# Optimization experiments

Hardware: AMD Instinct MI355X
Metric: run time of the kernel (lower is better)

The kernel has to match this reference:

```python
import jax, jax.numpy as jnp
import numpy as np

B, S, E, H, FFN, NQ = 4, 2048, 1024, 16, 4096, 8
DK = E // H
EPS = 1e-5


def setup_inputs() -> dict:
    key = jax.random.key(0)
    ks = jax.random.split(key, 8)
    x = jax.random.normal(ks[0], (B, S, E), dtype=jnp.float32)
    theta = jax.random.normal(ks[1], (NQ,), dtype=jnp.float32)  # RY angles
    w1 = jax.random.normal(ks[2], (FFN, NQ), dtype=jnp.float32) / np.sqrt(NQ)
    b1 = jnp.zeros((FFN,), dtype=jnp.float32)
    w2 = jax.random.normal(ks[3], (E, FFN), dtype=jnp.float32) / np.sqrt(FFN)
    b2 = jnp.zeros((E,), dtype=jnp.float32)
    gamma1 = jnp.ones((E,), dtype=jnp.float32)
    beta1 = jnp.zeros((E,), dtype=jnp.float32)
    gamma2 = jnp.ones((E,), dtype=jnp.float32)
    beta2 = jnp.zeros((E,), dtype=jnp.float32)
    return {"x": x, "theta": theta, "w1": w1, "b1": b1, "w2": w2, "b2": b2,
            "gamma1": gamma1, "beta1": beta1, "gamma2": gamma2, "beta2": beta2}


def _layernorm(h, g, b):
    mu = jnp.mean(h, axis=-1, keepdims=True)
    var = jnp.mean(jnp.square(h - mu), axis=-1, keepdims=True)
    return (h - mu) * jax.lax.rsqrt(var + EPS) * g + b


def _attention(x):
    # q = k = v = separate_heads(x); no projection weights in the original.
    q = x.reshape(B, S, H, DK).transpose(0, 2, 1, 3)  # [B,H,S,DK]
    scores = jnp.einsum("bhqd,bhkd->bhqk", q, q) / np.sqrt(DK)
    probs = jax.nn.softmax(scores, axis=-1)
    out = jnp.einsum("bhqk,bhkd->bhqd", probs, q)
    return out.transpose(0, 2, 1, 3).reshape(B, S, E)


def _ffn_quantum(h, theta, w1, b1, w2, b2):
    # Per-token circuit: RX(x_i) then RY(theta_i) on independent qubits,
    # measure PauliZ -> <Z_i> = cos(x_i) * cos(theta_i). Batched over all tokens.
    qout = jnp.cos(h[..., :NQ]) * jnp.cos(theta)  # [B,S,NQ]
    hid = jax.nn.relu(jnp.einsum("bsq,fq->bsf", qout, w1) + b1)
    return jnp.einsum("bsf,ef->bse", hid, w2) + b2


def reference(x, theta, w1, b1, w2, b2, gamma1, beta1, gamma2, beta2):
    attn_out = _attention(x)
    h = _layernorm(x + attn_out, gamma1, beta1)
    ffn_out = _ffn_quantum(h, theta, w1, b1, w2, b2)
    return _layernorm(h + ffn_out, gamma2, beta2)
```

## Files before the change

kernel.cpp:

```cpp
#include <hip/hip_runtime.h>


#define Bq 4
#define Sq 2048
#define Eq 1024
#define Hq 16
#define DKq 64
#define FFNq 4096
#define NQq 8
#define LOG2E 1.44269504f

typedef unsigned int u32;
typedef unsigned short u16;
typedef _Float16 f16;
typedef f16 f16x8 __attribute__((ext_vector_type(8)));
typedef __fp16 fp16x2 __attribute__((ext_vector_type(2)));
typedef float f32x4 __attribute__((ext_vector_type(4)));
typedef u32 u32x2 __attribute__((ext_vector_type(2)));
typedef u32 u32x4 __attribute__((ext_vector_type(4)));

#if __has_builtin(__builtin_amdgcn_exp2f)
#define EXP2F __builtin_amdgcn_exp2f
#else
#define EXP2F exp2f
#endif

#define MFMA(a, b, c) __builtin_amdgcn_mfma_f32_16x16x32_f16((a), (b), (c), 0, 0, 0)

#define GLL(g, l)                                                          \
  __builtin_amdgcn_global_load_lds(                                        \
      (const __attribute__((address_space(1))) u32*)(g),                   \
      (__attribute__((address_space(3))) u32*)(l), 16, 0, 0)

__device__ __forceinline__ u16 f2h(float x) {
  f16 t = (f16)x;
  return __builtin_bit_cast(u16, t);
}
__device__ __forceinline__ float h2f(u16 w) {
  return (float)__builtin_bit_cast(f16, w);
}
#if __has_builtin(__builtin_amdgcn_cvt_pkrtz)
__device__ __forceinline__ u32 pkrtz(float a, float b) {
  fp16x2 r = __builtin_amdgcn_cvt_pkrtz(a, b);
  return __builtin_bit_cast(u32, r);
}
#else
__device__ __forceinline__ u32 pkrtz(float a, float b) {
  return (u32)f2h(a) | ((u32)f2h(b) << 16);
}
#endif

__device__ __forceinline__ void swap32(u32 a, u32 b, u32& r0, u32& r1) {
#if __has_builtin(__builtin_amdgcn_permlane32_swap)
  u32x2 r = __builtin_amdgcn_permlane32_swap(a, b, false, false);
  r0 = r[0];
  r1 = r[1];
#else
  u32 ax = (u32)__shfl_xor((int)a, 32);
  u32 bx = (u32)__shfl_xor((int)b, 32);
  const bool lo = (threadIdx.x & 32) == 0;
  r0 = lo ? a : bx;
  r1 = lo ? ax : b;
#endif
}

union F8 { f16x8 v; u32 w[4]; u16 h[8]; f16 e[8]; };

__global__ void k_cvt(const float* __restrict__ src, uint4* __restrict__ dst, int n8) {
  int i = blockIdx.x * 256 + threadIdx.x;
  if (i >= n8) return;
  const float4* s = (const float4*)src + 2 * (long)i;
  float4 a = s[0], b = s[1];
  uint4 r;
  r.x = pkrtz(a.x, a.y);
  r.y = pkrtz(a.z, a.w);
  r.z = pkrtz(b.x, b.y);
  r.w = pkrtz(b.z, b.w);
  dst[i] = r;
}

__global__ void k_prep(const float* __restrict__ x, u16* __restrict__ xh,
                       u16* __restrict__ xt) {
  __shared__ u16 tile[64 * 72];
  const int tid = threadIdx.x;
  const int bx = blockIdx.x;
  const int sb = bx & 31, bh = bx >> 5;
  const int b = bh >> 4, h = bh & 15;
  const int s0 = sb * 64;
  const int r = tid >> 2, cq = tid & 3;
  const float* xp = x + ((long)(b * Sq + s0 + r)) * Eq + h * 64 + cq * 16;
  float4 f0 = ((const float4*)xp)[0], f1 = ((const float4*)xp)[1];
  float4 f2 = ((const float4*)xp)[2], f3 = ((const float4*)xp)[3];
  u32 w[8];
  w[0] = pkrtz(f0.x, f0.y); w[1] = pkrtz(f0.z, f0.w);
  w[2] = pkrtz(f1.x, f1.y); w[3] = pkrtz(f1.z, f1.w);
  w[4] = pkrtz(f2.x, f2.y); w[5] = pkrtz(f2.z, f2.w);
  w[6] = pkrtz(f3.x, f3.y); w[7] = pkrtz(f3.z, f3.w);
  uint4* xo = (uint4*)(xh + ((long)(b * Sq + s0 + r)) * Eq + h * 64 + cq * 16);
  xo[0] = make_uint4(w[0], w[1], w[2], w[3]);
  xo[1] = make_uint4(w[4], w[5], w[6], w[7]);
  uint4* tp = (uint4*)(tile + r * 72 + cq * 16);
  tp[0] = make_uint4(w[0], w[1], w[2], w[3]);
  tp[1] = make_uint4(w[4], w[5], w[6], w[7]);
  __syncthreads();
  const int d = tid >> 2, rq = tid & 3;
  u32 o[8];
#pragma unroll
  for (int i = 0; i < 8; ++i) {
    u32 lo = tile[(rq * 16 + 2 * i) * 72 + d];
    u32 hi = tile[(rq * 16 + 2 * i + 1) * 72 + d];
    o[i] = lo | (hi << 16);
  }
  uint4* to = (uint4*)(xt + ((long)(bh * 64 + d)) * Sq + s0 + rq * 16);
  to[0] = make_uint4(o[0], o[1], o[2], o[3]);
  to[1] = make_uint4(o[4], o[5], o[6], o[7]);
}

__global__ __launch_bounds__(512, 4) void k_attn(const u16* __restrict__ xh,
                                                 const u16* __restrict__ xt,
                                                 u16* __restrict__ attn) {
  __shared__ __align__(16) u16 lds[16384];

  const int tid = threadIdx.x;
  const int wave = tid >> 6, lane = tid & 63;
  const int n = lane & 15, quad = lane >> 4;
  const bool quadEven = (quad & 1) == 0;

  const int bx = blockIdx.x;
  const int qb = bx >> 6, bh = bx & 63;
  const int b = bh >> 4, h = bh & 15;

  const u16* xh_bh = xh + (long)b * Sq * Eq + h * 64;
  const u16* xt_bh = xt + (long)bh * 64 * Sq;

  const float SC = 0.125f * LOG2E;
  F8 qf[2][2];
  float shift[2], lrow[2] = {0.f, 0.f};
#pragma unroll
  for (int nt = 0; nt < 2; ++nt) {
    const int q = qb * 256 + wave * 32 + nt * 16 + n;
    const u16* qp = xh_bh + (long)q * Eq + quad * 8;
    F8 a, c;
    a.v = *(const f16x8*)qp;
    c.v = *(const f16x8*)(qp + 32);
    float s2 = 0.f;
#pragma unroll
    for (int i = 0; i < 8; ++i) {
      float va = (float)a.e[i], vc = (float)c.e[i];
      s2 += va * va + vc * vc;
      qf[nt][0].e[i] = a.e[i] * (f16)SC;
      qf[nt][1].e[i] = c.e[i] * (f16)SC;
    }
    s2 += __shfl_xor(s2, 16);
    s2 += __shfl_xor(s2, 32);
    shift[nt] = SC * s2;
  }

  const int r8 = lane >> 3;
  const int cl = (lane & 7) ^ r8;
  const u16* gK = xh_bh + (long)(wave * 8 + r8) * Eq + cl * 8;
  const u16* gV = xt_bh + (long)(wave * 8 + r8) * Sq + cl * 8;
  const int lK = wave * 512;
  const int lV = 4096 + wave * 512;

  u16* cur = lds;
  u16* nxt = lds + 8192;

  GLL(gK, cur + lK);
  GLL(gV, cur + lV);
  gK += 64 * Eq;
  gV += 64;

  f32x4 O[2][4] = {};

  for (int kb = 0; kb < Sq / 64; ++kb) {
    __syncthreads();
    if (kb < Sq / 64 - 1) {
      GLL(gK, nxt + lK);
      GLL(gV, nxt + lV);
      gK += 64 * Eq;
      gV += 64;
    }
    u16* Kl = cur;
    u16* Vt = cur + 4096;

    f32x4 ST[2][4];
#pragma unroll
    for (int nt = 0; nt < 2; ++nt) {
      const float ms = -shift[nt];
#pragma unroll
      for (int mt = 0; mt < 4; ++mt) {
        ST[nt][mt][0] = ms; ST[nt][mt][1] = ms;
        ST[nt][mt][2] = ms; ST[nt][mt][3] = ms;
      }
    }
    __builtin_amdgcn_s_setprio(1);
#pragma unroll
    for (int mt = 0; mt < 4; ++mt) {
#pragma unroll
      for (int c = 0; c < 2; ++c) {
        f16x8 af = *(const f16x8*)(Kl + (mt * 16 + n) * 64 +
                                   (((c * 4 + quad) ^ (n & 7)) * 8));
#pragma unroll
        for (int nt = 0; nt < 2; ++nt)
          ST[nt][mt] = MFMA(af, qf[nt][c].v, ST[nt][mt]);
      }
    }
    __builtin_amdgcn_s_setprio(0);

    f16x8 pfr[2][2];
#pragma unroll
    for (int nt = 0; nt < 2; ++nt) {
      u32 pk[8];
      float ls = 0.f;
#pragma unroll
      for (int mt = 0; mt < 4; ++mt) {
        float p0 = EXP2F(ST[nt][mt][0]);
        float p1 = EXP2F(ST[nt][mt][1]);
        float p2 = EXP2F(ST[nt][mt][2]);
        float p3 = EXP2F(ST[nt][mt][3]);
        ls += (p0 + p1) + (p2 + p3);
        pk[2 * mt] = pkrtz(p0, p1);
        pk[2 * mt + 1] = pkrtz(p2, p3);
      }
      lrow[nt] += ls;
#pragma unroll
      for (int c = 0; c < 2; ++c) {
        u32 r00, r10, r01, r11;
        swap32(pk[4 * c + 0], pk[4 * c + 2], r00, r10);
        swap32(pk[4 * c + 1], pk[4 * c + 3], r01, r11);
        u32 U0 = quadEven ? r10 : r00;
        u32 U1 = quadEven ? r11 : r01;
        u32 Ux0 = (u32)__shfl_xor((int)U0, 16);
        u32 Ux1 = (u32)__shfl_xor((int)U1, 16);
        u32x4 wv;
        wv[0] = quadEven ? r00 : Ux0;
        wv[1] = quadEven ? r01 : Ux1;
        wv[2] = quadEven ? Ux0 : r10;
        wv[3] = quadEven ? Ux1 : r11;
        pfr[nt][c] = __builtin_bit_cast(f16x8, wv);
      }
    }

    __builtin_amdgcn_s_setprio(1);
#pragma unroll
    for (int c = 0; c < 2; ++c) {
      const int pc = ((c * 4 + quad) ^ (n & 7)) * 8;
#pragma unroll
      for (int dt = 0; dt < 4; ++dt) {
        f16x8 vf = *(const f16x8*)(Vt + (dt * 16 + n) * 64 + pc);
#pragma unroll
        for (int nt = 0; nt < 2; ++nt) O[nt][dt] = MFMA(vf, pfr[nt][c], O[nt][dt]);
      }
    }
    __builtin_amdgcn_s_setprio(0);
    u16* t = cur; cur = nxt; nxt = t;
  }

#pragma unroll
  for (int nt = 0; nt < 2; ++nt) {
    float l = lrow[nt];
    l += __shfl_xor(l, 16);
    l += __shfl_xor(l, 32);
    const float inv = 1.0f / l;
    const int q = qb * 256 + wave * 32 + nt * 16 + n;
    u16* op = attn + (long)b * Sq * Eq + (long)q * Eq + h * 64;
#pragma unroll
    for (int dt = 0; dt < 4; ++dt) {
      u32 w0 = pkrtz(O[nt][dt][0] * inv, O[nt][dt][1] * inv);
      u32 w1 = pkrtz(O[nt][dt][2] * inv, O[nt][dt][3] * inv);
      *(uint2*)(op + dt * 16 + quad * 4) = make_uint2(w0, w1);
    }
  }
}

__global__ void k_ln1(const u16* __restrict__ xh, const u16* __restrict__ attn,
                      const float* __restrict__ g, const float* __restrict__ be,
                      const float* __restrict__ theta, u16* __restrict__ hout,
                      u16* __restrict__ qout) {
  const long t = blockIdx.x;
  const int tid = threadIdx.x;
  uint2 xw = ((const uint2*)(xh + t * Eq))[tid];
  uint2 aw = ((const uint2*)(attn + t * Eq))[tid];
  float v0 = h2f(xw.x & 0xffff) + h2f(aw.x & 0xffff);
  float v1 = h2f(xw.x >> 16) + h2f(aw.x >> 16);
  float v2 = h2f(xw.y & 0xffff) + h2f(aw.y & 0xffff);
  float v3 = h2f(xw.y >> 16) + h2f(aw.y >> 16);
  float s = (v0 + v1) + (v2 + v3);
  float s2 = v0 * v0 + v1 * v1 + v2 * v2 + v3 * v3;
#pragma unroll
  for (int o = 1; o < 64; o <<= 1) {
    s += __shfl_xor(s, o);
    s2 += __shfl_xor(s2, o);
  }
  __shared__ float red[8];
  const int wv = tid >> 6, ln = tid & 63;
  if (ln == 0) { red[wv] = s; red[4 + wv] = s2; }
  __syncthreads();
  s = red[0] + red[1] + red[2] + red[3];
  s2 = red[4] + red[5] + red[6] + red[7];
  const float mu = s * (1.f / Eq);
  const float var = s2 * (1.f / Eq) - mu * mu;
  const float rstd = rsqrtf(var + 1e-5f);
  float4 gv = ((const float4*)g)[tid];
  float4 bv = ((const float4*)be)[tid];
  float o0 = (v0 - mu) * rstd * gv.x + bv.x;
  float o1 = (v1 - mu) * rstd * gv.y + bv.y;
  float o2 = (v2 - mu) * rstd * gv.z + bv.z;
  float o3 = (v3 - mu) * rstd * gv.w + bv.w;
  ((uint2*)(hout + t * Eq))[tid] = make_uint2(pkrtz(o0, o1), pkrtz(o2, o3));
  if (tid < 2) {
    float hv[4] = {o0, o1, o2, o3};
    float q[4];
#pragma unroll
    for (int i = 0; i < 4; ++i) q[i] = cosf(hv[i]) * cosf(theta[tid * 4 + i]);
    *(uint2*)(qout + t * NQq + tid * 4) = make_uint2(pkrtz(q[0], q[1]), pkrtz(q[2], q[3]));
  }
}

__global__ void k_hid(const u16* __restrict__ qout, const float* __restrict__ w1,
                      const float* __restrict__ b1, u16* __restrict__ hid) {
  __shared__ float qs[256][8];
  const int tid = threadIdx.x;
  const int fb = blockIdx.x & 63, tb = blockIdx.x >> 6;
  const int f0 = fb * 64, t0 = tb * 256;
  {
    uint4 qw = *(const uint4*)(qout + (long)(t0 + tid) * NQq);
    qs[tid][0] = h2f(qw.x & 0xffff); qs[tid][1] = h2f(qw.x >> 16);
    qs[tid][2] = h2f(qw.y & 0xffff); qs[tid][3] = h2f(qw.y >> 16);
    qs[tid][4] = h2f(qw.z & 0xffff); qs[tid][5] = h2f(qw.z >> 16);
    qs[tid][6] = h2f(qw.w & 0xffff); qs[tid][7] = h2f(qw.w >> 16);
  }
  __syncthreads();
  const int wave = tid >> 6, lane = tid & 63;
  const int f = f0 + lane;
  const float4* wp = (const float4*)(w1 + (long)f * NQq);
  float4 wa = wp[0], wb = wp[1];
  const float bb = b1[f];
  const int trow = wave * 64;
  u16* op = hid + (long)(t0 + trow) * FFNq + f;
#pragma unroll 4
  for (int i = 0; i < 64; ++i) {
    const float* q = qs[trow + i];
    float acc = bb + q[0] * wa.x + q[1] * wa.y + q[2] * wa.z + q[3] * wa.w +
                q[4] * wb.x + q[5] * wb.y + q[6] * wb.z + q[7] * wb.w;
    acc = fmaxf(acc, 0.f);
    op[(long)i * FFNq] = f2h(acc);
  }
}

__global__ __launch_bounds__(256, 2) void k_gemm(const u16* __restrict__ Ah,
                                                 const u16* __restrict__ Bh,
                                                 u16* __restrict__ C) {
  __shared__ __align__(16) u16 lds[32768];
  const int tid = threadIdx.x;
  const int wave = tid >> 6, lane = tid & 63;
  const int n = lane & 15, quad = lane >> 4;
  const int wm = wave >> 1, wn = wave & 1;
  const int m0 = (blockIdx.x >> 3) * 128;
  const int n0 = (blockIdx.x & 7) * 128;
  const int r8 = lane >> 3;
  const int cl = (lane & 7) ^ r8;

  const u16* gA[4];
  const u16* gB[4];
  int lA[4], lB[4];
#pragma unroll
  for (int j = 0; j < 4; ++j) {
    const int row = wave * 32 + j * 8;
    gA[j] = Ah + (long)(m0 + row + r8) * FFNq + cl * 8;
    gB[j] = Bh + (long)(n0 + row + r8) * FFNq + cl * 8;
    lA[j] = row * 64;
    lB[j] = 8192 + row * 64;
  }

  u16* cur = lds;
  u16* nxt = lds + 16384;

#pragma unroll
  for (int j = 0; j < 4; ++j) {
    GLL(gA[j], cur + lA[j]);
    GLL(gB[j], cur + lB[j]);
    gA[j] += 64;
    gB[j] += 64;
  }

  f32x4 acc[4][4] = {};
  for (int it = 0; it < FFNq / 64; ++it) {
    __syncthreads();
    if (it < FFNq / 64 - 1) {
#pragma unroll
      for (int j = 0; j < 4; ++j) {
        GLL(gA[j], nxt + lA[j]);
        GLL(gB[j], nxt + lB[j]);
        gA[j] += 64;
        gB[j] += 64;
      }
    }
    u16* La = cur;
    u16* Lb = cur + 8192;
#pragma unroll
    for (int c = 0; c < 2; ++c) {
      f16x8 af[4], bf[4];
#pragma unroll
      for (int i = 0; i < 4; ++i) {
        const int ra = wm * 64 + i * 16 + n;
        const int rb = wn * 64 + i * 16 + n;
        af[i] = *(const f16x8*)(La + ra * 64 + (((c * 4 + quad) ^ (n & 7)) * 8));
        bf[i] = *(const f16x8*)(Lb + rb * 64 + (((c * 4 + quad) ^ (n & 7)) * 8));
      }
#pragma unroll
      for (int i = 0; i < 4; ++i)
#pragma unroll
        for (int j = 0; j < 4; ++j) acc[i][j] = MFMA(af[i], bf[j], acc[i][j]);
    }
    u16* t = cur; cur = nxt; nxt = t;
  }
#pragma unroll
  for (int i = 0; i < 4; ++i) {
    const int row = m0 + wm * 64 + i * 16 + quad * 4;
#pragma unroll
    for (int j = 0; j < 4; ++j) {
      u16* cp = C + (long)row * Eq + n0 + wn * 64 + j * 16 + n;
      cp[0] = f2h(acc[i][j][0]);
      cp[Eq] = f2h(acc[i][j][1]);
      cp[2 * Eq] = f2h(acc[i][j][2]);
      cp[3 * Eq] = f2h(acc[i][j][3]);
    }
  }
}

__global__ void k_ln2(const u16* __restrict__ hin, const u16* __restrict__ ffn,
                      const float* __restrict__ b2, const float* __restrict__ g,
                      const float* __restrict__ be, float* __restrict__ out) {
  const long t = blockIdx.x;
  const int tid = threadIdx.x;
  uint2 hw = ((const uint2*)(hin + t * Eq))[tid];
  uint2 fw = ((const uint2*)(ffn + t * Eq))[tid];
  float4 b2v = ((const float4*)b2)[tid];
  float v0 = h2f(hw.x & 0xffff) + h2f(fw.x & 0xffff) + b2v.x;
  float v1 = h2f(hw.x >> 16) + h2f(fw.x >> 16) + b2v.y;
  float v2 = h2f(hw.y & 0xffff) + h2f(fw.y & 0xffff) + b2v.z;
  float v3 = h2f(hw.y >> 16) + h2f(fw.y >> 16) + b2v.w;
  float s = (v0 + v1) + (v2 + v3);
  float s2 = v0 * v0 + v1 * v1 + v2 * v2 + v3 * v3;
#pragma unroll
  for (int o = 1; o < 64; o <<= 1) {
    s += __shfl_xor(s, o);
    s2 += __shfl_xor(s2, o);
  }
  __shared__ float red[8];
  const int wv = tid >> 6, ln = tid & 63;
  if (ln == 0) { red[wv] = s; red[4 + wv] = s2; }
  __syncthreads();
  s = red[0] + red[1] + red[2] + red[3];
  s2 = red[4] + red[5] + red[6] + red[7];
  const float mu = s * (1.f / Eq);
  const float var = s2 * (1.f / Eq) - mu * mu;
  const float rstd = rsqrtf(var + 1e-5f);
  float4 gv = ((const float4*)g)[tid];
  float4 bv = ((const float4*)be)[tid];
  float4 o;
  o.x = (v0 - mu) * rstd * gv.x + bv.x;
  o.y = (v1 - mu) * rstd * gv.y + bv.y;
  o.z = (v2 - mu) * rstd * gv.z + bv.z;
  o.w = (v3 - mu) * rstd * gv.w + bv.w;
  ((float4*)(out + t * Eq))[tid] = o;
}

extern "C" void kernel_launch(void* const* d_in, const int* in_sizes, int n_in,
                              void* d_out, int out_size, void* d_ws, size_t ws_size,
                              hipStream_t stream) {
  const float* x = (const float*)d_in[0];
  const float* theta = (const float*)d_in[1];
  const float* w1 = (const float*)d_in[2];
  const float* b1 = (const float*)d_in[3];
  const float* w2 = (const float*)d_in[4];
  const float* b2 = (const float*)d_in[5];
  const float* g1 = (const float*)d_in[6];
  const float* be1 = (const float*)d_in[7];
  const float* g2 = (const float*)d_in[8];
  const float* be2 = (const float*)d_in[9];
  float* out = (float*)d_out;

  char* ws = (char*)d_ws;
  u16* attn = (u16*)(ws);
  u16* h = (u16*)(ws + 16777216);
  u16* xh = (u16*)(ws + 33554432);
  u16* xt = (u16*)(ws + 50331648);
  u16* ffn = (u16*)(ws + 67108864);
  u16* hid = (u16*)(ws + 83886080);
  u16* w2h = (u16*)(ws + 150994944);
  u16* qout = (u16*)(ws + 159383552);

  k_prep<<<Bq * Hq * (Sq / 64), 256, 0, stream>>>(x, xh, xt);
  k_cvt<<<2048, 256, 0, stream>>>(w2, (uint4*)w2h, (Eq * FFNq) / 8);
  k_attn<<<Bq * Hq * (Sq / 256), 512, 0, stream>>>(xh, xt, attn);
  k_ln1<<<Bq * Sq, 256, 0, stream>>>(xh, attn, g1, be1, theta, h, qout);
  k_hid<<<(Bq * Sq / 256) * (FFNq / 64), 256, 0, stream>>>(qout, w1, b1, hid);
  k_gemm<<<(Bq * Sq / 128) * (Eq / 128), 256, 0, stream>>>(hid, w2h, ffn);
  k_ln2<<<Bq * Sq, 256, 0, stream>>>(h, ffn, b2, g2, be2, out);
}
```

Measured before the change: 319.1 us.

## Switch attention kernel to 32x32x16 MFMA tiles

Rewrites the attention inner loop to use 32x32x16 f16 MFMA instead of 16x16x32, so each wave handles a 32-query tile with a single accumulator layout. This removes the cross-lane shuffles and selects previously needed to rearrange P into the B-operand layout, and halves the per-row reduction shuffles. The LDS read patterns, swizzle indexing and output store layout are remapped to match. Larger MFMA tiles need fewer instructions for the same work, but the 16-element accumulators raise register pressure at the 4-blocks-per-CU launch bound.

```diff
diff --git a/kernel.cpp b/kernel.cpp
--- a/kernel.cpp
+++ b/kernel.cpp
@@ -16,6 +16,7 @@
 typedef f16 f16x8 __attribute__((ext_vector_type(8)));
 typedef __fp16 fp16x2 __attribute__((ext_vector_type(2)));
 typedef float f32x4 __attribute__((ext_vector_type(4)));
+typedef float f32x16 __attribute__((ext_vector_type(16)));
 typedef u32 u32x2 __attribute__((ext_vector_type(2)));
 typedef u32 u32x4 __attribute__((ext_vector_type(4)));
 
@@ -26,6 +27,7 @@
 #endif
 
 #define MFMA(a, b, c) __builtin_amdgcn_mfma_f32_16x16x32_f16((a), (b), (c), 0, 0, 0)
+#define MFMA32(a, b, c) __builtin_amdgcn_mfma_f32_32x32x16_f16((a), (b), (c), 0, 0, 0)
 
 #define GLL(g, l)                                                          \
   __builtin_amdgcn_global_load_lds(                                        \
@@ -123,8 +125,8 @@
 
   const int tid = threadIdx.x;
   const int wave = tid >> 6, lane = tid & 63;
-  const int n = lane & 15, quad = lane >> 4;
-  const bool quadEven = (quad & 1) == 0;
+  const int col = lane & 31;
+  const int hh = lane >> 5;
 
   const int bx = blockIdx.x;
   const int qb = bx >> 6, bh = bx & 63;
@@ -134,27 +136,27 @@
   const u16* xt_bh = xt + (long)bh * 64 * Sq;
 
   const float SC = 0.125f * LOG2E;
-  F8 qf[2][2];
-  float shift[2], lrow[2] = {0.f, 0.f};
-#pragma unroll
-  for (int nt = 0; nt < 2; ++nt) {
-    const int q = qb * 256 + wave * 32 + nt * 16 + n;
-    const u16* qp = xh_bh + (long)q * Eq + quad * 8;
-    F8 a, c;
-    a.v = *(const f16x8*)qp;
-    c.v = *(const f16x8*)(qp + 32);
+  const int q = qb * 256 + wave * 32 + col;
+  F8 qf[4];
+  float shift;
+  {
+    const u16* qp = xh_bh + (long)q * Eq + hh * 8;
     float s2 = 0.f;
 #pragma unroll
-    for (int i = 0; i < 8; ++i) {
-      float va = (float)a.e[i], vc = (float)c.e[i];
-      s2 += va * va + vc * vc;
-      qf[nt][0].e[i] = a.e[i] * (f16)SC;
-      qf[nt][1].e[i] = c.e[i] * (f16)SC;
-    }
-    s2 += __shfl_xor(s2, 16);
+    for (int st = 0; st < 4; ++st) {
+      F8 a;
+      a.v = *(const f16x8*)(qp + st * 16);
+#pragma unroll
+      for (int i = 0; i < 8; ++i) {
+        float v = (float)a.e[i];
+        s2 += v * v;
+        qf[st].e[i] = a.e[i] * (f16)SC;
+      }
+    }
     s2 += __shfl_xor(s2, 32);
-    shift[nt] = SC * s2;
-  }
+    shift = SC * s2;
+  }
+  float lrow = 0.f;
 
   const int r8 = lane >> 3;
   const int cl = (lane & 7) ^ r8;
@@ -171,7 +173,7 @@
   gK += 64 * Eq;
   gV += 64;
 
-  f32x4 O[2][4] = {};
+  f32x16 O[2] = {};
 
   for (int kb = 0; kb < Sq / 64; ++kb) {
     __syncthreads();
@@ -184,92 +186,77 @@
     u16* Kl = cur;
     u16* Vt = cur + 4096;
 
-    f32x4 ST[2][4];
-#pragma unroll
-    for (int nt = 0; nt < 2; ++nt) {
-      const float ms = -shift[nt];
-#pragma unroll
-      for (int mt = 0; mt < 4; ++mt) {
-        ST[nt][mt][0] = ms; ST[nt][mt][1] = ms;
-        ST[nt][mt][2] = ms; ST[nt][mt][3] = ms;
-      }
-    }
-    __builtin_amdgcn_s_setprio(1);
-#pragma unroll
-    for (int mt = 0; mt < 4; ++mt) {
-#pragma unroll
-      for (int c = 0; c < 2; ++c) {
-        f16x8 af = *(const f16x8*)(Kl + (mt * 16 + n) * 64 +
-                                   (((c * 4 + quad) ^ (n & 7)) * 8));
-#pragma unroll
-        for (int nt = 0; nt < 2; ++nt)
-          ST[nt][mt] = MFMA(af, qf[nt][c].v, ST[nt][mt]);
-      }
-    }
-    __builtin_amdgcn_s_setprio(0);
-
-    f16x8 pfr[2][2];
-#pragma unroll
-    for (int nt = 0; nt < 2; ++nt) {
+    f16x8 pf[4];
+#pragma unroll
+    for (int kt = 0; kt < 2; ++kt) {
+      f32x16 ST;
+#pragma unroll
+      for (int r = 0; r < 16; ++r) ST[r] = -shift;
+      const int krow = kt * 32 + col;
+      const u16* kp = Kl + krow * 64;
+      const int sw = krow & 7;
+      __builtin_amdgcn_s_setprio(1);
+#pragma unroll
+      for (int st = 0; st < 4; ++st) {
+        f16x8 af = *(const f16x8*)(kp + ((2 * st + hh) ^ sw) * 8);
+        ST = MFMA32(af, qf[st].v, ST);
+      }
+      __builtin_amdgcn_s_setprio(0);
+
       u32 pk[8];
       float ls = 0.f;
 #pragma unroll
-      for (int mt = 0; mt < 4; ++mt) {
-        float p0 = EXP2F(ST[nt][mt][0]);
-        float p1 = EXP2F(ST[nt][mt][1]);
-        float p2 = EXP2F(ST[nt][mt][2]);
-        float p3 = EXP2F(ST[nt][mt][3]);
+      for (int j = 0; j < 4; ++j) {
+        float p0 = EXP2F(ST[4 * j + 0]);
+        float p1 = EXP2F(ST[4 * j + 1]);
+        float p2 = EXP2F(ST[4 * j + 2]);
+        float p3 = EXP2F(ST[4 * j + 3]);
         ls += (p0 + p1) + (p2 + p3);
-        pk[2 * mt] = pkrtz(p0, p1);
-        pk[2 * mt + 1] = pkrtz(p2, p3);
-      }
-      lrow[nt] += ls;
-#pragma unroll
-      for (int c = 0; c < 2; ++c) {
-        u32 r00, r10, r01, r11;
-        swap32(pk[4 * c + 0], pk[4 * c + 2], r00, r10);
-        swap32(pk[4 * c + 1], pk[4 * c + 3], r01, r11);
-        u32 U0 = quadEven ? r10 : r00;
-        u32 U1 = quadEven ? r11 : r01;
-        u32 Ux0 = (u32)__shfl_xor((int)U0, 16);
-        u32 Ux1 = (u32)__shfl_xor((int)U1, 16);
+        pk[2 * j] = pkrtz(p0, p1);
+        pk[2 * j + 1] = pkrtz(p2, p3);
+      }
+      lrow += ls;
+#pragma unroll
+      for (int s = 0; s < 2; ++s) {
+        u32 e0, e1, e2, e3;
+        swap32(pk[4 * s + 0], pk[4 * s + 2], e0, e2);
+        swap32(pk[4 * s + 1], pk[4 * s + 3], e1, e3);
         u32x4 wv;
-        wv[0] = quadEven ? r00 : Ux0;
-        wv[1] = quadEven ? r01 : Ux1;
-        wv[2] = quadEven ? Ux0 : r10;
-        wv[3] = quadEven ? Ux1 : r11;
-        pfr[nt][c] = __builtin_bit_cast(f16x8, wv);
+        wv[0] = e0;
+        wv[1] = e1;
+        wv[2] = e2;
+        wv[3] = e3;
+        pf[kt * 2 + s] = __builtin_bit_cast(f16x8, wv);
       }
     }
 
     __builtin_amdgcn_s_setprio(1);
 #pragma unroll
-    for (int c = 0; c < 2; ++c) {
-      const int pc = ((c * 4 + quad) ^ (n & 7)) * 8;
-#pragma unroll
-      for (int dt = 0; dt < 4; ++dt) {
-        f16x8 vf = *(const f16x8*)(Vt + (dt * 16 + n) * 64 + pc);
-#pragma unroll
-        for (int nt = 0; nt < 2; ++nt) O[nt][dt] = MFMA(vf, pfr[nt][c], O[nt][dt]);
+    for (int dt = 0; dt < 2; ++dt) {
+      const int vrow = dt * 32 + col;
+      const u16* vp = Vt + vrow * 64;
+      const int sw = vrow & 7;
+#pragma unroll
+      for (int ks = 0; ks < 4; ++ks) {
+        f16x8 vf = *(const f16x8*)(vp + ((2 * ks + hh) ^ sw) * 8);
+        O[dt] = MFMA32(vf, pf[ks], O[dt]);
       }
     }
     __builtin_amdgcn_s_setprio(0);
     u16* t = cur; cur = nxt; nxt = t;
   }
 
-#pragma unroll
-  for (int nt = 0; nt < 2; ++nt) {
-    float l = lrow[nt];
-    l += __shfl_xor(l, 16);
-    l += __shfl_xor(l, 32);
-    const float inv = 1.0f / l;
-    const int q = qb * 256 + wave * 32 + nt * 16 + n;
-    u16* op = attn + (long)b * Sq * Eq + (long)q * Eq + h * 64;
-#pragma unroll
-    for (int dt = 0; dt < 4; ++dt) {
-      u32 w0 = pkrtz(O[nt][dt][0] * inv, O[nt][dt][1] * inv);
-      u32 w1 = pkrtz(O[nt][dt][2] * inv, O[nt][dt][3] * inv);
-      *(uint2*)(op + dt * 16 + quad * 4) = make_uint2(w0, w1);
+  float l = lrow + __shfl_xor(lrow, 32);
+  const float inv = 1.0f / l;
+  u16* op = attn + (long)b * Sq * Eq + (long)q * Eq + h * 64;
+#pragma unroll
+  for (int dt = 0; dt < 2; ++dt) {
+#pragma unroll
+    for (int j = 0; j < 4; ++j) {
+      const int d = dt * 32 + 8 * j + 4 * hh;
+      u32 w0 = pkrtz(O[dt][4 * j + 0] * inv, O[dt][4 * j + 1] * inv);
+      u32 w1 = pkrtz(O[dt][4 * j + 2] * inv, O[dt][4 * j + 3] * inv);
+      *(uint2*)(op + d) = make_uint2(w0, w1);
     }
   }
 }
```

Measured after the change: 315.1 us. Within noise of the previous version (-1.2%).
